# Optimization experiments

Hardware: AMD Instinct MI355X
Metric: run time of the kernel (lower is better)

Reference implementation:

```python
import jax, jax.numpy as jnp
import numpy as np

N_NODE = 4096   # nodes per graph (generalized from hardcoded 55)
IN_DIM = 200    # input_dim, forced by attn1 in_channel=200
OUT_DIM = 200   # output_dim, forced equal to input_dim by GRU_gate shapes
N_HEADS = 8     # forced by attn2 in_channel 1600 = 8*200
SEQ_LEN = 4
HID = 200       # hid_units default


def _glorot(k, shape):
    r = np.sqrt(6.0 / (shape[0] + shape[1])).astype(np.float32)
    return jax.random.uniform(k, shape, jnp.float32, -r, r)


def setup_inputs() -> dict:
    key = jax.random.key(0)
    ks = jax.random.split(key, 32)
    inp = {}
    mask = jax.random.bernoulli(ks[0], 0.01, (SEQ_LEN, N_NODE, N_NODE))
    inp['adjs'] = jax.random.uniform(ks[1], (SEQ_LEN, N_NODE, N_NODE), jnp.float32) * mask
    inp['feats'] = jax.random.normal(ks[2], (SEQ_LEN, N_NODE, IN_DIM), jnp.float32)
    inp['p_covss'] = jnp.zeros((SEQ_LEN,), jnp.float32)  # passed but unused in original
    # per-head weight_vars, randn(output_dim, input_dim) in original call()
    inp['init_wv'] = jax.random.normal(ks[3], (N_HEADS, OUT_DIM, IN_DIM), jnp.float32)
    # attn1 (shared across all heads): conv1d(k=1) == linear
    inp['W1'] = _glorot(ks[4], (HID, IN_DIM)); inp['b1'] = jnp.zeros((HID,), jnp.float32)
    inp['a11'] = _glorot(ks[5], (HID, 1))[:, 0]; inp['a11b'] = jnp.zeros((), jnp.float32)
    inp['a12'] = _glorot(ks[6], (HID, 1))[:, 0]; inp['a12b'] = jnp.zeros((), jnp.float32)
    # attn2
    inp['W2'] = _glorot(ks[7], (OUT_DIM, N_HEADS * HID)); inp['b2'] = jnp.zeros((OUT_DIM,), jnp.float32)
    inp['a21'] = _glorot(ks[8], (OUT_DIM, 1))[:, 0]; inp['a21b'] = jnp.zeros((), jnp.float32)
    inp['a22'] = _glorot(ks[9], (OUT_DIM, 1))[:, 0]; inp['a22b'] = jnp.zeros((), jnp.float32)
    # GRU gates (reset/update/htilda), reduce=True since n_node != input_dim
    for i, g in enumerate(['r', 'u', 'h']):
        inp['W' + g] = _glorot(ks[10 + 4 * i], (N_NODE, OUT_DIM))
        inp['U' + g] = _glorot(ks[11 + 4 * i], (OUT_DIM, OUT_DIM))
        inp['P' + g] = _glorot(ks[12 + 4 * i], (IN_DIM, N_NODE))
        inp['b' + g] = jnp.zeros((IN_DIM, OUT_DIM), jnp.float32)
    return inp


def reference(adjs, feats, p_covss, init_wv, W1, b1, a11, a11b, a12, a12b,
              W2, b2, a21, a21b, a22, a22b,
              Wr, Ur, Pr, br, Wu, Uu, Pu, bu, Wh, Uh, Ph, bh):
    def gat(x):  # x: [N, IN_DIM]
        fts = x @ W1.T + b1                                   # [N, HID]
        # logits f_1 + f_2^T on [N,1,1] stays [N,1,1]; softmax over the
        # singleton dim is identically 1 -> attention is degenerate.
        s = jax.nn.leaky_relu((fts @ a11 + a11b) + (fts @ a12 + a12b), 0.01)
        coefs = jnp.ones_like(s)                              # softmax([N,1,1], dim=1)
        h = jax.nn.elu(coefs[:, None] * fts)                  # [N, HID]
        hcat = jnp.tile(h, (1, N_HEADS))                      # heads share attn1 -> identical
        fts2 = hcat @ W2.T + b2                               # [N, OUT_DIM]
        s2 = jax.nn.leaky_relu((fts2 @ a21 + a21b) + (fts2 @ a22 + a22b), 0.01)
        coefs2 = jnp.ones_like(s2)
        out = jax.nn.elu(coefs2[:, None] * fts2)              # [N, OUT_DIM]
        # torch: out.view(nb_classes, -1).T then softmax(dim=1), then view(-1, out_dim)
        logits = jnp.reshape(out, (OUT_DIM, N_NODE)).T        # memory reinterpretation, not transpose
        return jax.nn.softmax(logits, axis=1)                 # [N, OUT_DIM]

    embeds = jax.vmap(gat)(feats)                             # [T, N, OUT_DIM]

    def gru_step(wv, adj):  # wv: [H, OUT_DIM, IN_DIM=OUT_DIM], adj: [N, N]
        # head-independent sparse propagation bases, one per gate
        gr = Pr @ (adj @ Wr) + br                             # [IN_DIM, OUT_DIM]
        gu = Pu @ (adj @ Wu) + bu
        gh = Ph @ (adj @ Wh) + bh
        r = jax.nn.sigmoid(gr + wv @ Ur)                      # [H, 200, 200]
        u = jax.nn.sigmoid(gu + wv @ Uu)
        hcap = jnp.tanh(gh + (r * wv) @ Uh)
        return (1.0 - u) * wv + u * hcap, None

    final_wv, _ = jax.lax.scan(gru_step, init_wv, adjs[1:])   # evolve over t=1..T-1
    return embeds, final_wv
```

## Files before the change

### kernel.cpp

```cpp
#include <hip/hip_runtime.h>
#include <hip/hip_bf16.h>
#include <math.h>

typedef __hip_bfloat16 bf16;
typedef __attribute__((ext_vector_type(8))) short short8;
typedef __attribute__((ext_vector_type(4))) float f32x4;

#define N_NODE 4096
#define DIM 200
#define NH 8
#define SEQ 4
#define TLDA 40

__device__ __forceinline__ float eluf(float x) { return x > 0.f ? x : expm1f(x); }
__device__ __forceinline__ float sigm(float x) { return 1.f / (1.f + expf(-x)); }

template<bool ISB>
__device__ __forceinline__ float ldv(const void* p, size_t i) {
    if (ISB) return __bfloat162float(((const bf16*)p)[i]);
    else     return ((const float*)p)[i];
}
template<bool ISB>
__device__ __forceinline__ void stv(void* p, size_t i, float v) {
    if (ISB) ((bf16*)p)[i] = __float2bfloat16(v);
    else     ((float*)p)[i] = v;
}
__device__ __forceinline__ float bflo(unsigned u) { return __uint_as_float((u & 0xffffu) << 16); }
__device__ __forceinline__ float bfhi(unsigned u) { return __uint_as_float(u & 0xffff0000u); }
__device__ __forceinline__ short f2bs(float v) {
    bf16 h = __float2bfloat16(v);
    return *(short*)&h;
}

__global__ void k_detect(const void* feats, int* flag) {
    __shared__ int cnt;
    if (threadIdx.x == 0) cnt = 0;
    __syncthreads();
    const unsigned short* u = (const unsigned short*)feats;
    unsigned short v = u[2 * threadIdx.x];
    int e = (v >> 7) & 0xFF;
    if (e >= 100 && e <= 140) atomicAdd(&cnt, 1);
    __syncthreads();
    if (threadIdx.x == 0) *flag = (cnt >= 128) ? 1 : 0;
}


template<bool AISB>
__device__ __forceinline__ void ldA8(const void* A, int lda, int arow, bool rowOK,
                                     int kk, int K, float* la) {
    if (rowOK && kk + 8 <= K) {
        if (AISB) {
            const unsigned short* ap = (const unsigned short*)A + (size_t)arow * lda + kk;
            uint4 u = *(const uint4*)ap;
            la[0] = bflo(u.x); la[1] = bfhi(u.x);
            la[2] = bflo(u.y); la[3] = bfhi(u.y);
            la[4] = bflo(u.z); la[5] = bfhi(u.z);
            la[6] = bflo(u.w); la[7] = bfhi(u.w);
        } else {
            const float* ap = (const float*)A + (size_t)arow * lda + kk;
            float4 f0 = *(const float4*)ap;
            float4 f1 = *(const float4*)(ap + 4);
            la[0] = f0.x; la[1] = f0.y; la[2] = f0.z; la[3] = f0.w;
            la[4] = f1.x; la[5] = f1.y; la[6] = f1.z; la[7] = f1.w;
        }
    } else {
#pragma unroll
        for (int j = 0; j < 8; j++)
            la[j] = (rowOK && kk + j < K) ? ldv<AISB>(A, (size_t)arow * lda + kk + j) : 0.f;
    }
}
template<bool BISB>
__device__ __forceinline__ void ldB8(const void* B, int gcol, bool colOK,
                                     int kk, int K, float* lb) {
#pragma unroll
    for (int j = 0; j < 8; j++)
        lb[j] = (colOK && kk + j < K) ? ldv<BISB>(B, (size_t)(kk + j) * DIM + gcol) : 0.f;
}

template<int EPI, bool AISB, bool BISB>
__device__ void mgemm(const void* A, int lda, const void* B, int M, int K,
                      int kbeg, int kend, const float* X1, const float* X2,
                      float* C, int row0, int c0, const int* fl, void* out2) {
    const int N = DIM;
    int tid = threadIdx.x;
    int wave = tid >> 6, lane = tid & 63;
    int m16 = lane & 15, q = lane >> 4;
    __shared__ short As[64 * TLDA];
    __shared__ short Bs[64 * TLDA];
    int s_row = tid >> 2;
    int s_k   = (tid & 3) * 8;
    int b_col = tid & 63;
    int b_kg  = (tid >> 6) * 8;
    int arow = row0 + s_row;
    bool rowOK = arow < M;
    int gcol = c0 + b_col;
    bool colOK = gcol < N;
    float la[8], lb[8];
    ldA8<AISB>(A, lda, arow, rowOK, kbeg + s_k, K, la);
    ldB8<BISB>(B, gcol, colOK, kbeg + b_kg, K, lb);
    f32x4 acc[4] = {};
    for (int k0 = kbeg; k0 < kend; k0 += 32) {
        __syncthreads();
        short8 a8, b8;
#pragma unroll
        for (int j = 0; j < 8; j++) { a8[j] = f2bs(la[j]); b8[j] = f2bs(lb[j]); }
        *(short8*)&As[s_row * TLDA + s_k] = a8;
        *(short8*)&Bs[b_col * TLDA + b_kg] = b8;
        __syncthreads();
        int kn = k0 + 32;
        if (kn < kend) {
            ldA8<AISB>(A, lda, arow, rowOK, kn + s_k, K, la);
            ldB8<BISB>(B, gcol, colOK, kn + b_kg, K, lb);
        }
        short8 bf = *(short8*)&Bs[(wave * 16 + m16) * TLDA + q * 8];
#pragma unroll
        for (int r = 0; r < 4; r++) {
            short8 af = *(short8*)&As[(r * 16 + m16) * TLDA + q * 8];
            acc[r] = __builtin_amdgcn_mfma_f32_16x16x32_bf16(af, bf, acc[r], 0, 0, 0);
        }
    }
    int colw = c0 + wave * 16 + m16;
    if (colw >= N) return;
#pragma unroll
    for (int r = 0; r < 4; r++) {
        int rowb = row0 + r * 16 + q * 4;
#pragma unroll
        for (int reg = 0; reg < 4; reg++) {
            int row = rowb + reg;
            if (row >= M) continue;
            float v = acc[r][reg];
            size_t ci = (size_t)row * 200 + colw;
            if (EPI == 0) {
                C[ci] = eluf(v + X1[colw]);
            } else if (EPI == 3) {
                int a200 = row - (row / 200) * 200;
                float uu = X2[ci];
                float hc = tanhf(X1[a200 * 200 + colw] + v);
                float nv = (1.f - uu) * C[ci] + uu * hc;
                C[ci] = nv;
                if (out2) {
                    size_t oo = (size_t)SEQ * N_NODE * DIM + ci;
                    if (*fl) stv<true>(out2, oo, nv); else stv<false>(out2, oo, nv);
                }
            } else {
                atomicAdd(&C[ci], v);
            }
        }
    }
}

__global__ __launch_bounds__(256) void k_gemm_e12(const float* A,
        const float* Br, const float* Bu, const float* Gr, const float* Gu,
        float* rw, float* u) {
    const int M = NH * DIM, K = DIM, N = DIM;
    int row0 = blockIdx.y * 64, c0 = blockIdx.x * 64;
    int tid = threadIdx.x;
    int wave = tid >> 6, lane = tid & 63;
    int m16 = lane & 15, q = lane >> 4;
    __shared__ short As[64 * TLDA];
    __shared__ short Bsr[64 * TLDA];
    __shared__ short Bsu[64 * TLDA];
    int s_row = tid >> 2;
    int s_k   = (tid & 3) * 8;
    int b_col = tid & 63;
    int b_kg  = (tid >> 6) * 8;
    int arow = row0 + s_row;
    bool rowOK = arow < M;
    int gcol = c0 + b_col;
    bool colOK = gcol < N;
    float la[8], lbr[8], lbu[8];
    ldA8<false>(A, K, arow, rowOK, s_k, K, la);
    ldB8<false>(Br, gcol, colOK, b_kg, K, lbr);
    ldB8<false>(Bu, gcol, colOK, b_kg, K, lbu);
    f32x4 accR[4] = {}, accU[4] = {};
    for (int k0 = 0; k0 < K; k0 += 32) {
        __syncthreads();
        short8 a8, r8, u8;
#pragma unroll
        for (int j = 0; j < 8; j++) {
            a8[j] = f2bs(la[j]); r8[j] = f2bs(lbr[j]); u8[j] = f2bs(lbu[j]);
        }
        *(short8*)&As[s_row * TLDA + s_k] = a8;
        *(short8*)&Bsr[b_col * TLDA + b_kg] = r8;
        *(short8*)&Bsu[b_col * TLDA + b_kg] = u8;
        __syncthreads();
        int kn = k0 + 32;
        if (kn < K) {
            ldA8<false>(A, K, arow, rowOK, kn + s_k, K, la);
            ldB8<false>(Br, gcol, colOK, kn + b_kg, K, lbr);
            ldB8<false>(Bu, gcol, colOK, kn + b_kg, K, lbu);
        }
        short8 bfr = *(short8*)&Bsr[(wave * 16 + m16) * TLDA + q * 8];
        short8 bfu = *(short8*)&Bsu[(wave * 16 + m16) * TLDA + q * 8];
#pragma unroll
        for (int r = 0; r < 4; r++) {
            short8 af = *(short8*)&As[(r * 16 + m16) * TLDA + q * 8];
            accR[r] = __builtin_amdgcn_mfma_f32_16x16x32_bf16(af, bfr, accR[r], 0, 0, 0);
            accU[r] = __builtin_amdgcn_mfma_f32_16x16x32_bf16(af, bfu, accU[r], 0, 0, 0);
        }
    }
    int colw = c0 + wave * 16 + m16;
    if (colw >= N) return;
#pragma unroll
    for (int r = 0; r < 4; r++) {
        int rowb = row0 + r * 16 + q * 4;
#pragma unroll
        for (int reg = 0; reg < 4; reg++) {
            int row = rowb + reg;
            if (row >= M) continue;
            int a200 = row - (row / 200) * 200;
            size_t ci = (size_t)row * 200 + colw;
            rw[ci] = sigm(Gr[a200 * 200 + colw] + accR[r][reg]) * A[ci];
            u[ci]  = sigm(Gu[a200 * 200 + colw] + accU[r][reg]);
        }
    }
}

__global__ __launch_bounds__(256) void k_gemm_e0(const int* fl, int useIsb,
        const void* A, int lda, const float* B, int M, int K,
        const float* bias, float* C) {
    int row0 = blockIdx.y * 64, c0 = blockIdx.x * 64;
    if (useIsb && *fl)
        mgemm<0, true , false>(A, lda, B, M, K, 0, K, bias, nullptr, C, row0, c0, nullptr, nullptr);
    else
        mgemm<0, false, false>(A, lda, B, M, K, 0, K, bias, nullptr, C, row0, c0, nullptr, nullptr);
}
__global__ __launch_bounds__(256) void k_gemm_e3(const float* A, const float* B,
        const float* G0, const float* U, float* WV, const int* fl, void* out2) {
    mgemm<3, false, false>(A, DIM, B, NH * DIM, DIM, 0, DIM, G0, U, WV,
                           blockIdx.y * 64, blockIdx.x * 64, fl, out2);
}
__global__ __launch_bounds__(256) void k_pggemm(const int* fl,
        const void* P0, const void* P1, const void* P2,
        const bf16* AWb, float* G) {
    int z = blockIdx.z;
    int sg = z >> 3, split = z & 7;
    int g = sg - (sg / 3) * 3;
    const void* A = (g == 0) ? P0 : (g == 1) ? P1 : P2;
    const void* B = AWb + (size_t)sg * N_NODE * DIM;
    float* C = G + (size_t)sg * DIM * DIM;
    int row0 = blockIdx.y * 64, c0 = blockIdx.x * 64;
    int kbeg = split * (N_NODE / 8), kend = kbeg + N_NODE / 8;
    if (*fl) mgemm<4, true , true>(A, N_NODE, B, DIM, N_NODE, kbeg, kend, nullptr, nullptr, C, row0, c0, nullptr, nullptr);
    else     mgemm<4, false, true>(A, N_NODE, B, DIM, N_NODE, kbeg, kend, nullptr, nullptr, C, row0, c0, nullptr, nullptr);
}

template<bool ISB>
__device__ void prep_body(const void* W1, const void* b1, const void* W2, const void* b2,
                          const void* Ur, const void* Uu, const void* Uh,
                          const void* br, const void* bu, const void* bh,
                          const void* iwv, const void* Wr, const void* Wu, const void* Wh,
                          float* W1t, float* W2t, float* b1f, float* b2f,
                          float* Utf, float* wv, float* G, unsigned short* Wcat) {
    int idx = blockIdx.x * 256 + threadIdx.x;
    if (idx < 40000) {
        int k = idx / 200, n = idx % 200;
        W1t[idx] = ldv<ISB>(W1, (size_t)n * 200 + k);
    } else if (idx < 80000) {
        int r = idx - 40000;
        int k = r / 200, n = r % 200;
        float s = 0.f;
        for (int h = 0; h < NH; h++) s += ldv<ISB>(W2, (size_t)n * 1600 + h * 200 + k);
        W2t[r] = s;
    } else if (idx < 80512) {
        int j = idx - 80000;
        if (j < 256)      b1f[j] = (j < 200) ? ldv<ISB>(b1, j) : 0.f;
        else              b2f[j - 256] = (j - 256 < 200) ? ldv<ISB>(b2, j - 256) : 0.f;
    } else if (idx < 200512) {
        int j = idx - 80512;
        int g = j / 40000, r = j - g * 40000;
        const void* U = (g == 0) ? Ur : (g == 1) ? Uu : Uh;
        Utf[j] = ldv<ISB>(U, r);
    } else if (idx < 520512) {
        wv[idx - 200512] = ldv<ISB>(iwv, idx - 200512);
    } else if (idx < 880512) {
        int j = idx - 520512;
        int sg = j / 40000, r = j - sg * 40000;
        int g = sg - (sg / 3) * 3;
        const void* bb = (g == 0) ? br : (g == 1) ? bu : bh;
        G[j] = ldv<ISB>(bb, r);
    } else {
        int j = idx - 880512;
        if (j < 4096 * 600) {
            int k = j / 600, c = j - k * 600;
            int g = (c < 200) ? 0 : (c < 400 ? 1 : 2);
            int o = c - g * 200;
            const void* W = (g == 0) ? Wr : (g == 1) ? Wu : Wh;
            bf16 v = __float2bfloat16(ldv<ISB>(W, (size_t)k * 200 + o));
            Wcat[(size_t)k * 608 + c] = *(unsigned short*)&v;
        }
    }
}
__global__ void k_prep(const int* fl, const void* W1, const void* b1, const void* W2,
                       const void* b2, const void* Ur, const void* Uu, const void* Uh,
                       const void* br, const void* bu, const void* bh, const void* iwv,
                       const void* Wr, const void* Wu, const void* Wh,
                       float* W1t, float* W2t, float* b1f, float* b2f,
                       float* Utf, float* wv, float* G, unsigned short* Wcat) {
    if (*fl) prep_body<true >(W1, b1, W2, b2, Ur, Uu, Uh, br, bu, bh, iwv, Wr, Wu, Wh,
                              W1t, W2t, b1f, b2f, Utf, wv, G, Wcat);
    else     prep_body<false>(W1, b1, W2, b2, Ur, Uu, Uh, br, bu, bh, iwv, Wr, Wu, Wh,
                              W1t, W2t, b1f, b2f, Utf, wv, G, Wcat);
}

template<bool ISB>
__device__ void softmax_body(const float* O, void* out) {
    __shared__ float tile[200 * 65];
    __shared__ float pm[4 * 64];
    __shared__ float ps[4 * 64];
    __shared__ float sm_m[64];
    __shared__ float sm_inv[64];
    int t = blockIdx.y;
    int i0 = blockIdx.x * 64;
    const float* ob = O + (size_t)t * N_NODE * DIM;
    int tid = threadIdx.x;
    for (int idx = tid; idx < 200 * 64; idx += 256) {
        int j = idx >> 6, c = idx & 63;
        tile[j * 65 + c] = ob[(size_t)j * N_NODE + i0 + c];
    }
    __syncthreads();
    int g = tid >> 6, lane = tid & 63;
    int j0 = g * 50, j1 = j0 + 50;
    float mp = -1e30f;
    for (int j = j0; j < j1; j++) mp = fmaxf(mp, tile[j * 65 + lane]);
    pm[g * 64 + lane] = mp;
    __syncthreads();
    if (tid < 64)
        sm_m[tid] = fmaxf(fmaxf(pm[tid], pm[64 + tid]), fmaxf(pm[128 + tid], pm[192 + tid]));
    __syncthreads();
    float mv = sm_m[lane];
    float sp = 0.f;
    for (int j = j0; j < j1; j++) {
        float e = expf(tile[j * 65 + lane] - mv);
        tile[j * 65 + lane] = e;
        sp += e;
    }
    ps[g * 64 + lane] = sp;
    __syncthreads();
    if (tid < 64)
        sm_inv[tid] = 1.f / (ps[tid] + ps[64 + tid] + ps[128 + tid] + ps[192 + tid]);
    __syncthreads();
    size_t ob2 = ((size_t)t * N_NODE + i0) * DIM;
    for (int idx = tid; idx < 64 * 200; idx += 256) {
        int il = idx / 200, j = idx - il * 200;
        stv<ISB>(out, ob2 + (size_t)il * DIM + j, tile[j * 65 + il] * sm_inv[il]);
    }
}
__global__ __launch_bounds__(256) void k_softmax(const int* fl, const float* O, void* out) {
    if (*fl) softmax_body<true>(O, out); else softmax_body<false>(O, out);
}

template<bool ISB>
__device__ void aw_body(const void* adjs, const unsigned short* Wcat, bf16* AWb) {
    int i = blockIdx.x;
    int s = blockIdx.y;
    size_t arow = ((size_t)(s + 1) * N_NODE + i) * N_NODE;
    __shared__ int   s_k[512];
    __shared__ float s_v[512];
    __shared__ int   s_cnt;
    int tid = threadIdx.x;
    if (tid == 0) s_cnt = 0;
    __syncthreads();
    float vals[16];
#pragma unroll
    for (int c = 0; c < 4; c++) {
        int col = c * 1024 + tid * 4;
        if (ISB) {
            ushort4 u = *(const ushort4*)((const unsigned short*)adjs + arow + col);
            vals[c*4+0] = __uint_as_float((unsigned)u.x << 16);
            vals[c*4+1] = __uint_as_float((unsigned)u.y << 16);
            vals[c*4+2] = __uint_as_float((unsigned)u.z << 16);
            vals[c*4+3] = __uint_as_float((unsigned)u.w << 16);
        } else {
            float4 f = *(const float4*)((const float*)adjs + arow + col);
            vals[c*4+0] = f.x; vals[c*4+1] = f.y; vals[c*4+2] = f.z; vals[c*4+3] = f.w;
        }
    }
#pragma unroll
    for (int q = 0; q < 16; q++) {
        if (vals[q] != 0.f) {
            int p = atomicAdd(&s_cnt, 1);
            if (p < 512) { s_k[p] = (q >> 2) * 1024 + tid * 4 + (q & 3); s_v[p] = vals[q]; }
        }
    }
    __syncthreads();
    int n = s_cnt < 512 ? s_cnt : 512;
    float a0 = 0.f, a1 = 0.f, d0 = 0.f, d1 = 0.f;
    bool hasB = (tid < 44);
    int offA = 2 * tid, offB = 512 + 2 * tid;
    int e = 0;
    for (; e + 4 <= n; e += 4) {
        int   k0 = s_k[e],   k1 = s_k[e+1], k2 = s_k[e+2], k3 = s_k[e+3];
        float v0 = s_v[e],   v1 = s_v[e+1], v2 = s_v[e+2], v3 = s_v[e+3];
        unsigned wa0 = *(const unsigned*)(Wcat + (size_t)k0 * 608 + offA);
        unsigned wa1 = *(const unsigned*)(Wcat + (size_t)k1 * 608 + offA);
        unsigned wa2 = *(const unsigned*)(Wcat + (size_t)k2 * 608 + offA);
        unsigned wa3 = *(const unsigned*)(Wcat + (size_t)k3 * 608 + offA);
        if (hasB) {
            unsigned wb0 = *(const unsigned*)(Wcat + (size_t)k0 * 608 + offB);
            unsigned wb1 = *(const unsigned*)(Wcat + (size_t)k1 * 608 + offB);
            unsigned wb2 = *(const unsigned*)(Wcat + (size_t)k2 * 608 + offB);
            unsigned wb3 = *(const unsigned*)(Wcat + (size_t)k3 * 608 + offB);
            d0 += v0*bflo(wb0) + v1*bflo(wb1) + v2*bflo(wb2) + v3*bflo(wb3);
            d1 += v0*bfhi(wb0) + v1*bfhi(wb1) + v2*bfhi(wb2) + v3*bfhi(wb3);
        }
        a0 += v0*bflo(wa0) + v1*bflo(wa1) + v2*bflo(wa2) + v3*bflo(wa3);
        a1 += v0*bfhi(wa0) + v1*bfhi(wa1) + v2*bfhi(wa2) + v3*bfhi(wa3);
    }
    for (; e < n; e++) {
        int k = s_k[e]; float v = s_v[e];
        unsigned wa = *(const unsigned*)(Wcat + (size_t)k * 608 + offA);
        a0 += v * bflo(wa); a1 += v * bfhi(wa);
        if (hasB) {
            unsigned wb = *(const unsigned*)(Wcat + (size_t)k * 608 + offB);
            d0 += v * bflo(wb); d1 += v * bfhi(wb);
        }
    }
    int gA = (offA < 200) ? 0 : (offA < 400 ? 1 : 2);
    int oA = offA - gA * 200;
    size_t wbase = ((size_t)(s * 3 + gA) * N_NODE + i) * DIM + oA;
    AWb[wbase]     = __float2bfloat16(a0);
    AWb[wbase + 1] = __float2bfloat16(a1);
    if (hasB) {
        int oB = offB - 400;
        size_t wb2 = ((size_t)(s * 3 + 2) * N_NODE + i) * DIM + oB;
        AWb[wb2]     = __float2bfloat16(d0);
        AWb[wb2 + 1] = __float2bfloat16(d1);
    }
}
__global__ __launch_bounds__(256) void k_aw(const int* fl, const void* adjs,
        const unsigned short* Wcat, bf16* AWb) {
    if (*fl) aw_body<true>(adjs, Wcat, AWb);
    else     aw_body<false>(adjs, Wcat, AWb);
}

extern "C" void kernel_launch(void* const* d_in, const int* in_sizes, int n_in,
                              void* d_out, int out_size, void* d_ws, size_t ws_size,
                              hipStream_t stream) {
    const void* adjs    = d_in[0];
    const void* feats   = d_in[1];
    const void* init_wv = d_in[3];
    const void* W1 = d_in[4];
    const void* b1 = d_in[5];
    const void* W2 = d_in[10];
    const void* b2 = d_in[11];
    const void* Wr = d_in[16];
    const void* Ur = d_in[17];
    const void* Pr = d_in[18];
    const void* br = d_in[19];
    const void* Wu = d_in[20];
    const void* Uu = d_in[21];
    const void* Pu = d_in[22];
    const void* bu = d_in[23];
    const void* Wh = d_in[24];
    const void* Uh = d_in[25];
    const void* Ph = d_in[26];
    const void* bh = d_in[27];

    int*   flag = (int*)d_ws;
    float* base = (float*)d_ws;
    unsigned short* Wcat = (unsigned short*)(base + 64);
    bf16*  AWb  = (bf16*)(base + 64 + 1245184);
    float* Hbuf = base + 64;
    float* Obuf = Hbuf + 3276800;
    float* W1t  = base + 6553664;
    float* W2t  = W1t + 40000;
    float* b1f  = W2t + 40000;
    float* b2f  = b1f + 256;
    float* ubuf = b2f + 256;
    float* rwbuf= ubuf + 320000;
    float* Utf  = rwbuf + 320000;
    float* G    = Utf + 120000;
    float* wv   = G + 360000;

    const int M = SEQ * N_NODE;

    k_detect<<<1, 256, 0, stream>>>(feats, flag);
    k_prep<<<(3338112 + 255) / 256, 256, 0, stream>>>(
        flag, W1, b1, W2, b2, Ur, Uu, Uh, br, bu, bh, init_wv, Wr, Wu, Wh,
        W1t, W2t, b1f, b2f, Utf, wv, G, Wcat);

    {
        dim3 g(N_NODE, 3);
        k_aw<<<g, 256, 0, stream>>>(flag, adjs, Wcat, AWb);
    }
    {
        dim3 g(4, 4, 72);
        k_pggemm<<<g, 256, 0, stream>>>(flag, Pr, Pu, Ph, AWb, G);
    }

    {
        dim3 g(4, M / 64);
        k_gemm_e0<<<g, 256, 0, stream>>>(flag, 1, feats, DIM, W1t, M, DIM, b1f, Hbuf);
        k_gemm_e0<<<g, 256, 0, stream>>>(flag, 0, Hbuf, DIM, W2t, M, DIM, b2f, Obuf);
    }
    {
        dim3 g(N_NODE / 64, SEQ);
        k_softmax<<<g, 256, 0, stream>>>(flag, Obuf, d_out);
    }

    {
        dim3 g(4, NH * DIM / 64);
        for (int s = 0; s < 3; s++) {
            const float* Gr = G + (size_t)(s * 3 + 0) * DIM * DIM;
            const float* Gu = G + (size_t)(s * 3 + 1) * DIM * DIM;
            const float* Gh = G + (size_t)(s * 3 + 2) * DIM * DIM;
            void* out2 = (s == 2) ? d_out : nullptr;
            k_gemm_e12<<<g, 256, 0, stream>>>(wv, Utf + 0, Utf + 40000, Gr, Gu, rwbuf, ubuf);
            k_gemm_e3<<<g, 256, 0, stream>>>(rwbuf, Utf + 80000, Gh, ubuf, wv, flag, out2);
        }
    }
}
```

Before: 671.4 us.

## Merge independent stages into heterogeneous kernels and replace split-K atomics with reduction

The sparse AW propagation and the first attention GEMM now share one launch, and the P·AW split-K GEMM shares one with the second attention GEMM. A third launch combines a deterministic reduction of the split-K partials with the softmax. Split-K partials go to a separate Gp buffer with plain stores instead of atomicAdd into G, and the workspace layout is moved so Hbuf no longer aliases Wcat/AWb. This cuts launch count and lets independent work fill the GPU together, at the cost of extra partial-buffer traffic and larger workspace.

```diff
diff --git a/kernel.cpp b/kernel.cpp
--- a/kernel.cpp
+++ b/kernel.cpp
@@ -43,7 +43,6 @@
     __syncthreads();
     if (threadIdx.x == 0) *flag = (cnt >= 128) ? 1 : 0;
 }
-
 
 template<bool AISB>
 __device__ __forceinline__ void ldA8(const void* A, int lda, int arow, bool rowOK,
@@ -143,9 +142,193 @@
                     if (*fl) stv<true>(out2, oo, nv); else stv<false>(out2, oo, nv);
                 }
             } else {
-                atomicAdd(&C[ci], v);
+                C[ci] = v;
             }
         }
+    }
+}
+
+template<bool ISB>
+__device__ void aw_body(const void* adjs, const unsigned short* Wcat, bf16* AWb,
+                        int i, int s) {
+    size_t arow = ((size_t)(s + 1) * N_NODE + i) * N_NODE;
+    __shared__ int   s_k[512];
+    __shared__ float s_v[512];
+    __shared__ int   s_cnt;
+    int tid = threadIdx.x;
+    if (tid == 0) s_cnt = 0;
+    __syncthreads();
+    float vals[16];
+#pragma unroll
+    for (int c = 0; c < 4; c++) {
+        int col = c * 1024 + tid * 4;
+        if (ISB) {
+            ushort4 u = *(const ushort4*)((const unsigned short*)adjs + arow + col);
+            vals[c*4+0] = __uint_as_float((unsigned)u.x << 16);
+            vals[c*4+1] = __uint_as_float((unsigned)u.y << 16);
+            vals[c*4+2] = __uint_as_float((unsigned)u.z << 16);
+            vals[c*4+3] = __uint_as_float((unsigned)u.w << 16);
+        } else {
+            float4 f = *(const float4*)((const float*)adjs + arow + col);
+            vals[c*4+0] = f.x; vals[c*4+1] = f.y; vals[c*4+2] = f.z; vals[c*4+3] = f.w;
+        }
+    }
+#pragma unroll
+    for (int q = 0; q < 16; q++) {
+        if (vals[q] != 0.f) {
+            int p = atomicAdd(&s_cnt, 1);
+            if (p < 512) { s_k[p] = (q >> 2) * 1024 + tid * 4 + (q & 3); s_v[p] = vals[q]; }
+        }
+    }
+    __syncthreads();
+    int n = s_cnt < 512 ? s_cnt : 512;
+    float a0 = 0.f, a1 = 0.f, d0 = 0.f, d1 = 0.f;
+    bool hasB = (tid < 44);
+    int offA = 2 * tid, offB = 512 + 2 * tid;
+    int e = 0;
+    for (; e + 4 <= n; e += 4) {
+        int   k0 = s_k[e],   k1 = s_k[e+1], k2 = s_k[e+2], k3 = s_k[e+3];
+        float v0 = s_v[e],   v1 = s_v[e+1], v2 = s_v[e+2], v3 = s_v[e+3];
+        unsigned wa0 = *(const unsigned*)(Wcat + (size_t)k0 * 608 + offA);
+        unsigned wa1 = *(const unsigned*)(Wcat + (size_t)k1 * 608 + offA);
+        unsigned wa2 = *(const unsigned*)(Wcat + (size_t)k2 * 608 + offA);
+        unsigned wa3 = *(const unsigned*)(Wcat + (size_t)k3 * 608 + offA);
+        if (hasB) {
+            unsigned wb0 = *(const unsigned*)(Wcat + (size_t)k0 * 608 + offB);
+            unsigned wb1 = *(const unsigned*)(Wcat + (size_t)k1 * 608 + offB);
+            unsigned wb2 = *(const unsigned*)(Wcat + (size_t)k2 * 608 + offB);
+            unsigned wb3 = *(const unsigned*)(Wcat + (size_t)k3 * 608 + offB);
+            d0 += v0*bflo(wb0) + v1*bflo(wb1) + v2*bflo(wb2) + v3*bflo(wb3);
+            d1 += v0*bfhi(wb0) + v1*bfhi(wb1) + v2*bfhi(wb2) + v3*bfhi(wb3);
+        }
+        a0 += v0*bflo(wa0) + v1*bflo(wa1) + v2*bflo(wa2) + v3*bflo(wa3);
+        a1 += v0*bfhi(wa0) + v1*bfhi(wa1) + v2*bfhi(wa2) + v3*bfhi(wa3);
+    }
+    for (; e < n; e++) {
+        int k = s_k[e]; float v = s_v[e];
+        unsigned wa = *(const unsigned*)(Wcat + (size_t)k * 608 + offA);
+        a0 += v * bflo(wa); a1 += v * bfhi(wa);
+        if (hasB) {
+            unsigned wb = *(const unsigned*)(Wcat + (size_t)k * 608 + offB);
+            d0 += v * bflo(wb); d1 += v * bfhi(wb);
+        }
+    }
+    int gA = (offA < 200) ? 0 : (offA < 400 ? 1 : 2);
+    int oA = offA - gA * 200;
+    size_t wbase = ((size_t)(s * 3 + gA) * N_NODE + i) * DIM + oA;
+    AWb[wbase]     = __float2bfloat16(a0);
+    AWb[wbase + 1] = __float2bfloat16(a1);
+    if (hasB) {
+        int oB = offB - 400;
+        size_t wb2 = ((size_t)(s * 3 + 2) * N_NODE + i) * DIM + oB;
+        AWb[wb2]     = __float2bfloat16(d0);
+        AWb[wb2 + 1] = __float2bfloat16(d1);
+    }
+}
+
+__global__ __launch_bounds__(256) void k_p2(const int* fl, const void* adjs,
+        const unsigned short* Wcat, bf16* AWb,
+        const void* feats, const float* W1t, const float* b1f, float* Hbuf) {
+    int b = blockIdx.x;
+    if (b < 12288) {
+        int i = b & (N_NODE - 1), s = b >> 12;
+        if (*fl) aw_body<true >(adjs, Wcat, AWb, i, s);
+        else     aw_body<false>(adjs, Wcat, AWb, i, s);
+    } else {
+        int t = b - 12288;
+        int row0 = (t >> 2) * 64, c0 = (t & 3) * 64;
+        if (*fl) mgemm<0, true , false>(feats, DIM, W1t, SEQ * N_NODE, DIM, 0, DIM,
+                                        b1f, nullptr, Hbuf, row0, c0, nullptr, nullptr);
+        else     mgemm<0, false, false>(feats, DIM, W1t, SEQ * N_NODE, DIM, 0, DIM,
+                                        b1f, nullptr, Hbuf, row0, c0, nullptr, nullptr);
+    }
+}
+
+__global__ __launch_bounds__(256) void k_p3(const int* fl,
+        const void* P0, const void* P1, const void* P2, const bf16* AWb, float* Gp,
+        const float* Hbuf, const float* W2t, const float* b2f, float* Obuf) {
+    int b = blockIdx.x;
+    if (b < 1152) {
+        int z = b >> 4, rem = b & 15;
+        int row0 = (rem >> 2) * 64, c0 = (rem & 3) * 64;
+        int sg = z >> 3, split = z & 7;
+        int g = sg - (sg / 3) * 3;
+        const void* A = (g == 0) ? P0 : (g == 1) ? P1 : P2;
+        const void* B = AWb + (size_t)sg * N_NODE * DIM;
+        float* C = Gp + (size_t)z * DIM * DIM;
+        int kbeg = split * (N_NODE / 8), kend = kbeg + N_NODE / 8;
+        if (*fl) mgemm<4, true , true>(A, N_NODE, B, DIM, N_NODE, kbeg, kend,
+                                       nullptr, nullptr, C, row0, c0, nullptr, nullptr);
+        else     mgemm<4, false, true>(A, N_NODE, B, DIM, N_NODE, kbeg, kend,
+                                       nullptr, nullptr, C, row0, c0, nullptr, nullptr);
+    } else {
+        int t = b - 1152;
+        int row0 = (t >> 2) * 64, c0 = (t & 3) * 64;
+        mgemm<0, false, false>(Hbuf, DIM, W2t, SEQ * N_NODE, DIM, 0, DIM,
+                               b2f, nullptr, Obuf, row0, c0, nullptr, nullptr);
+    }
+}
+
+template<bool ISB>
+__device__ void softmax_body(const float* O, void* out, int t, int i0) {
+    __shared__ float tile[200 * 65];
+    __shared__ float pm[4 * 64];
+    __shared__ float ps[4 * 64];
+    __shared__ float sm_m[64];
+    __shared__ float sm_inv[64];
+    const float* ob = O + (size_t)t * N_NODE * DIM;
+    int tid = threadIdx.x;
+    for (int idx = tid; idx < 200 * 64; idx += 256) {
+        int j = idx >> 6, c = idx & 63;
+        tile[j * 65 + c] = ob[(size_t)j * N_NODE + i0 + c];
+    }
+    __syncthreads();
+    int g = tid >> 6, lane = tid & 63;
+    int j0 = g * 50, j1 = j0 + 50;
+    float mp = -1e30f;
+    for (int j = j0; j < j1; j++) mp = fmaxf(mp, tile[j * 65 + lane]);
+    pm[g * 64 + lane] = mp;
+    __syncthreads();
+    if (tid < 64)
+        sm_m[tid] = fmaxf(fmaxf(pm[tid], pm[64 + tid]), fmaxf(pm[128 + tid], pm[192 + tid]));
+    __syncthreads();
+    float mv = sm_m[lane];
+    float sp = 0.f;
+    for (int j = j0; j < j1; j++) {
+        float e = expf(tile[j * 65 + lane] - mv);
+        tile[j * 65 + lane] = e;
+        sp += e;
+    }
+    ps[g * 64 + lane] = sp;
+    __syncthreads();
+    if (tid < 64)
+        sm_inv[tid] = 1.f / (ps[tid] + ps[64 + tid] + ps[128 + tid] + ps[192 + tid]);
+    __syncthreads();
+    size_t ob2 = ((size_t)t * N_NODE + i0) * DIM;
+    for (int idx = tid; idx < 64 * 200; idx += 256) {
+        int il = idx / 200, j = idx - il * 200;
+        stv<ISB>(out, ob2 + (size_t)il * DIM + j, tile[j * 65 + il] * sm_inv[il]);
+    }
+}
+
+__global__ __launch_bounds__(256) void k_p4(const int* fl, const float* Gp, float* G,
+                                            const float* Obuf, void* out) {
+    int b = blockIdx.x;
+    if (b < 1407) {
+        int idx = b * 256 + threadIdx.x;
+        if (idx < 9 * DIM * DIM) {
+            int sg = idx / (DIM * DIM), r = idx - sg * (DIM * DIM);
+            float s = 0.f;
+#pragma unroll
+            for (int sp = 0; sp < 8; sp++)
+                s += Gp[(size_t)(sg * 8 + sp) * DIM * DIM + r];
+            G[idx] += s;
+        }
+    } else {
+        int t = b - 1407;
+        int i0 = (t & 63) * 64, tt = t >> 6;
+        if (*fl) softmax_body<true >(Obuf, out, tt, i0);
+        else     softmax_body<false>(Obuf, out, tt, i0);
     }
 }
 
@@ -215,34 +398,10 @@
         }
     }
 }
-
-__global__ __launch_bounds__(256) void k_gemm_e0(const int* fl, int useIsb,
-        const void* A, int lda, const float* B, int M, int K,
-        const float* bias, float* C) {
-    int row0 = blockIdx.y * 64, c0 = blockIdx.x * 64;
-    if (useIsb && *fl)
-        mgemm<0, true , false>(A, lda, B, M, K, 0, K, bias, nullptr, C, row0, c0, nullptr, nullptr);
-    else
-        mgemm<0, false, false>(A, lda, B, M, K, 0, K, bias, nullptr, C, row0, c0, nullptr, nullptr);
-}
 __global__ __launch_bounds__(256) void k_gemm_e3(const float* A, const float* B,
         const float* G0, const float* U, float* WV, const int* fl, void* out2) {
     mgemm<3, false, false>(A, DIM, B, NH * DIM, DIM, 0, DIM, G0, U, WV,
                            blockIdx.y * 64, blockIdx.x * 64, fl, out2);
-}
-__global__ __launch_bounds__(256) void k_pggemm(const int* fl,
-        const void* P0, const void* P1, const void* P2,
-        const bf16* AWb, float* G) {
-    int z = blockIdx.z;
-    int sg = z >> 3, split = z & 7;
-    int g = sg - (sg / 3) * 3;
-    const void* A = (g == 0) ? P0 : (g == 1) ? P1 : P2;
-    const void* B = AWb + (size_t)sg * N_NODE * DIM;
-    float* C = G + (size_t)sg * DIM * DIM;
-    int row0 = blockIdx.y * 64, c0 = blockIdx.x * 64;
-    int kbeg = split * (N_NODE / 8), kend = kbeg + N_NODE / 8;
-    if (*fl) mgemm<4, true , true>(A, N_NODE, B, DIM, N_NODE, kbeg, kend, nullptr, nullptr, C, row0, c0, nullptr, nullptr);
-    else     mgemm<4, false, true>(A, N_NODE, B, DIM, N_NODE, kbeg, kend, nullptr, nullptr, C, row0, c0, nullptr, nullptr);
 }
 
 template<bool ISB>
@@ -303,137 +462,6 @@
                               W1t, W2t, b1f, b2f, Utf, wv, G, Wcat);
 }
 
-template<bool ISB>
-__device__ void softmax_body(const float* O, void* out) {
-    __shared__ float tile[200 * 65];
-    __shared__ float pm[4 * 64];
-    __shared__ float ps[4 * 64];
-    __shared__ float sm_m[64];
-    __shared__ float sm_inv[64];
-    int t = blockIdx.y;
-    int i0 = blockIdx.x * 64;
-    const float* ob = O + (size_t)t * N_NODE * DIM;
-    int tid = threadIdx.x;
-    for (int idx = tid; idx < 200 * 64; idx += 256) {
-        int j = idx >> 6, c = idx & 63;
-        tile[j * 65 + c] = ob[(size_t)j * N_NODE + i0 + c];
-    }
-    __syncthreads();
-    int g = tid >> 6, lane = tid & 63;
-    int j0 = g * 50, j1 = j0 + 50;
-    float mp = -1e30f;
-    for (int j = j0; j < j1; j++) mp = fmaxf(mp, tile[j * 65 + lane]);
-    pm[g * 64 + lane] = mp;
-    __syncthreads();
-    if (tid < 64)
-        sm_m[tid] = fmaxf(fmaxf(pm[tid], pm[64 + tid]), fmaxf(pm[128 + tid], pm[192 + tid]));
-    __syncthreads();
-    float mv = sm_m[lane];
-    float sp = 0.f;
-    for (int j = j0; j < j1; j++) {
-        float e = expf(tile[j * 65 + lane] - mv);
-        tile[j * 65 + lane] = e;
-        sp += e;
-    }
-    ps[g * 64 + lane] = sp;
-    __syncthreads();
-    if (tid < 64)
-        sm_inv[tid] = 1.f / (ps[tid] + ps[64 + tid] + ps[128 + tid] + ps[192 + tid]);
-    __syncthreads();
-    size_t ob2 = ((size_t)t * N_NODE + i0) * DIM;
-    for (int idx = tid; idx < 64 * 200; idx += 256) {
-        int il = idx / 200, j = idx - il * 200;
-        stv<ISB>(out, ob2 + (size_t)il * DIM + j, tile[j * 65 + il] * sm_inv[il]);
-    }
-}
-__global__ __launch_bounds__(256) void k_softmax(const int* fl, const float* O, void* out) {
-    if (*fl) softmax_body<true>(O, out); else softmax_body<false>(O, out);
-}
-
-template<bool ISB>
-__device__ void aw_body(const void* adjs, const unsigned short* Wcat, bf16* AWb) {
-    int i = blockIdx.x;
-    int s = blockIdx.y;
-    size_t arow = ((size_t)(s + 1) * N_NODE + i) * N_NODE;
-    __shared__ int   s_k[512];
-    __shared__ float s_v[512];
-    __shared__ int   s_cnt;
-    int tid = threadIdx.x;
-    if (tid == 0) s_cnt = 0;
-    __syncthreads();
-    float vals[16];
-#pragma unroll
-    for (int c = 0; c < 4; c++) {
-        int col = c * 1024 + tid * 4;
-        if (ISB) {
-            ushort4 u = *(const ushort4*)((const unsigned short*)adjs + arow + col);
-            vals[c*4+0] = __uint_as_float((unsigned)u.x << 16);
-            vals[c*4+1] = __uint_as_float((unsigned)u.y << 16);
-            vals[c*4+2] = __uint_as_float((unsigned)u.z << 16);
-            vals[c*4+3] = __uint_as_float((unsigned)u.w << 16);
-        } else {
-            float4 f = *(const float4*)((const float*)adjs + arow + col);
-            vals[c*4+0] = f.x; vals[c*4+1] = f.y; vals[c*4+2] = f.z; vals[c*4+3] = f.w;
-        }
-    }
-#pragma unroll
-    for (int q = 0; q < 16; q++) {
-        if (vals[q] != 0.f) {
-            int p = atomicAdd(&s_cnt, 1);
-            if (p < 512) { s_k[p] = (q >> 2) * 1024 + tid * 4 + (q & 3); s_v[p] = vals[q]; }
-        }
-    }
-    __syncthreads();
-    int n = s_cnt < 512 ? s_cnt : 512;
-    float a0 = 0.f, a1 = 0.f, d0 = 0.f, d1 = 0.f;
-    bool hasB = (tid < 44);
-    int offA = 2 * tid, offB = 512 + 2 * tid;
-    int e = 0;
-    for (; e + 4 <= n; e += 4) {
-        int   k0 = s_k[e],   k1 = s_k[e+1], k2 = s_k[e+2], k3 = s_k[e+3];
-        float v0 = s_v[e],   v1 = s_v[e+1], v2 = s_v[e+2], v3 = s_v[e+3];
-        unsigned wa0 = *(const unsigned*)(Wcat + (size_t)k0 * 608 + offA);
-        unsigned wa1 = *(const unsigned*)(Wcat + (size_t)k1 * 608 + offA);
-        unsigned wa2 = *(const unsigned*)(Wcat + (size_t)k2 * 608 + offA);
-        unsigned wa3 = *(const unsigned*)(Wcat + (size_t)k3 * 608 + offA);
-        if (hasB) {
-            unsigned wb0 = *(const unsigned*)(Wcat + (size_t)k0 * 608 + offB);
-            unsigned wb1 = *(const unsigned*)(Wcat + (size_t)k1 * 608 + offB);
-            unsigned wb2 = *(const unsigned*)(Wcat + (size_t)k2 * 608 + offB);
-            unsigned wb3 = *(const unsigned*)(Wcat + (size_t)k3 * 608 + offB);
-            d0 += v0*bflo(wb0) + v1*bflo(wb1) + v2*bflo(wb2) + v3*bflo(wb3);
-            d1 += v0*bfhi(wb0) + v1*bfhi(wb1) + v2*bfhi(wb2) + v3*bfhi(wb3);
-        }
-        a0 += v0*bflo(wa0) + v1*bflo(wa1) + v2*bflo(wa2) + v3*bflo(wa3);
-        a1 += v0*bfhi(wa0) + v1*bfhi(wa1) + v2*bfhi(wa2) + v3*bfhi(wa3);
-    }
-    for (; e < n; e++) {
-        int k = s_k[e]; float v = s_v[e];
-        unsigned wa = *(const unsigned*)(Wcat + (size_t)k * 608 + offA);
-        a0 += v * bflo(wa); a1 += v * bfhi(wa);
-        if (hasB) {
-            unsigned wb = *(const unsigned*)(Wcat + (size_t)k * 608 + offB);
-            d0 += v * bflo(wb); d1 += v * bfhi(wb);
-        }
-    }
-    int gA = (offA < 200) ? 0 : (offA < 400 ? 1 : 2);
-    int oA = offA - gA * 200;
-    size_t wbase = ((size_t)(s * 3 + gA) * N_NODE + i) * DIM + oA;
-    AWb[wbase]     = __float2bfloat16(a0);
-    AWb[wbase + 1] = __float2bfloat16(a1);
-    if (hasB) {
-        int oB = offB - 400;
-        size_t wb2 = ((size_t)(s * 3 + 2) * N_NODE + i) * DIM + oB;
-        AWb[wb2]     = __float2bfloat16(d0);
-        AWb[wb2 + 1] = __float2bfloat16(d1);
-    }
-}
-__global__ __launch_bounds__(256) void k_aw(const int* fl, const void* adjs,
-        const unsigned short* Wcat, bf16* AWb) {
-    if (*fl) aw_body<true>(adjs, Wcat, AWb);
-    else     aw_body<false>(adjs, Wcat, AWb);
-}
-
 extern "C" void kernel_launch(void* const* d_in, const int* in_sizes, int n_in,
                               void* d_out, int out_size, void* d_ws, size_t ws_size,
                               hipStream_t stream) {
@@ -460,10 +488,10 @@
     int*   flag = (int*)d_ws;
     float* base = (float*)d_ws;
     unsigned short* Wcat = (unsigned short*)(base + 64);
-    bf16*  AWb  = (bf16*)(base + 64 + 1245184);
-    float* Hbuf = base + 64;
+    bf16*  AWb  = (bf16*)(base + 1245248);
+    float* Hbuf = base + 4931648;
     float* Obuf = Hbuf + 3276800;
-    float* W1t  = base + 6553664;
+    float* W1t  = base + 11485248;
     float* W2t  = W1t + 40000;
     float* b1f  = W2t + 40000;
     float* b2f  = b1f + 256;
@@ -472,32 +500,16 @@
     float* Utf  = rwbuf + 320000;
     float* G    = Utf + 120000;
     float* wv   = G + 360000;
-
-    const int M = SEQ * N_NODE;
+    float* Gp   = wv + 320000;
 
     k_detect<<<1, 256, 0, stream>>>(feats, flag);
     k_prep<<<(3338112 + 255) / 256, 256, 0, stream>>>(
         flag, W1, b1, W2, b2, Ur, Uu, Uh, br, bu, bh, init_wv, Wr, Wu, Wh,
         W1t, W2t, b1f, b2f, Utf, wv, G, Wcat);
 
-    {
-        dim3 g(N_NODE, 3);
-        k_aw<<<g, 256, 0, stream>>>(flag, adjs, Wcat, AWb);
-    }
-    {
-        dim3 g(4, 4, 72);
-        k_pggemm<<<g, 256, 0, stream>>>(flag, Pr, Pu, Ph, AWb, G);
-    }
-
-    {
-        dim3 g(4, M / 64);
-        k_gemm_e0<<<g, 256, 0, stream>>>(flag, 1, feats, DIM, W1t, M, DIM, b1f, Hbuf);
-        k_gemm_e0<<<g, 256, 0, stream>>>(flag, 0, Hbuf, DIM, W2t, M, DIM, b2f, Obuf);
-    }
-    {
-        dim3 g(N_NODE / 64, SEQ);
-        k_softmax<<<g, 256, 0, stream>>>(flag, Obuf, d_out);
-    }
+    k_p2<<<13312, 256, 0, stream>>>(flag, adjs, Wcat, AWb, feats, W1t, b1f, Hbuf);
+    k_p3<<<2176, 256, 0, stream>>>(flag, Pr, Pu, Ph, AWb, Gp, Hbuf, W2t, b2f, Obuf);
+    k_p4<<<1663, 256, 0, stream>>>(flag, Gp, G, Obuf, d_out);
 
     {
         dim3 g(4, NH * DIM / 64);
```

New measurement: 753.3 us. 1.12x slower.
